# Kernel tuning notes

Hardware: AMD Instinct MI355X
Metric: run time of the kernel (lower is better)

The kernel has to match this reference:

```python
import jax, jax.numpy as jnp
import numpy as np

# Architecture constants from Dense_test.__init__
N_HID = 200      # n
BRANCH = 8
IN_DIM = 120     # 40 * 3
N_OUT = 12
VTH = 1.0        # vth=1, dt=1 -> R*dt factor = 1

# Multi-gaussian surrogate-gradient spike (ActFun_adp from DH-SNN)
LENS, SCALE, HIGHT, GAMMA = 0.5, 6.0, 0.15, 0.5

@jax.custom_vjp
def spike_fn(v):
    return (v > 0).astype(v.dtype)

def _spike_fwd(v):
    return (v > 0).astype(v.dtype), v

def _gauss(x, mu, sigma):
    return jnp.exp(-((x - mu) ** 2) / (2.0 * sigma ** 2)) / (jnp.sqrt(2.0 * jnp.pi) * sigma)

def _spike_bwd(v, g):
    sg = (_gauss(v, 0.0, LENS) * (1.0 + HIGHT)
          - _gauss(v, LENS, SCALE * LENS) * HIGHT
          - _gauss(v, -LENS, SCALE * LENS) * HIGHT)
    return (g * sg * GAMMA,)

spike_fn.defvjp(_spike_fwd, _spike_bwd)


def make_branch_mask(rng, in_features, out_dim, branch):
    # Each output neuron's dendritic branches connect to disjoint random
    # subsets of (input + recurrent) lines.
    k = in_features // branch
    mask = np.zeros((out_dim * branch, in_features), np.float32)
    for i in range(out_dim):
        seq = rng.permutation(in_features)
        for j in range(branch):
            mask[i * branch + j, seq[j * k:(j + 1) * k]] = 1.0
    return jnp.asarray(mask)


def setup_inputs() -> dict:
    rng = np.random.default_rng(0)
    key = jax.random.key(0)
    ks = jax.random.split(key, 16)
    B, T = 1024, 101
    d = {"x": jax.random.normal(ks[0], (B, 3, T, 40), jnp.float32)}
    in_feats = [IN_DIM + N_HID, N_HID + N_HID, N_HID + N_HID]
    for li, in_f in enumerate(in_feats, start=1):
        mask = make_branch_mask(rng, in_f, N_HID, BRANCH)
        W = jax.random.normal(ks[li], (N_HID * BRANCH, in_f), jnp.float32) / np.sqrt(in_f)
        d[f"W{li}"] = W * mask   # mask is applied multiplicatively to dense weights
        d[f"b{li}"] = jnp.zeros((N_HID * BRANCH,), jnp.float32)
        d[f"tau_m{li}"] = jax.random.uniform(ks[li + 4], (N_HID,), jnp.float32, 0.0, 4.0)
        d[f"tau_n{li}"] = jax.random.uniform(ks[li + 8], (N_HID, BRANCH), jnp.float32, 0.0, 4.0)
    d["W4"] = jax.random.normal(ks[12], (N_OUT, N_HID), jnp.float32) / np.sqrt(N_HID)
    d["b4"] = jnp.zeros((N_OUT,), jnp.float32)
    d["tau_m4"] = jax.random.uniform(ks[13], (N_OUT,), jnp.float32, 0.0, 4.0)
    return d


def _forward(x, W1, b1, tau_m1, tau_n1, W2, b2, tau_m2, tau_n2,
             W3, b3, tau_m3, tau_n3, W4, b4, tau_m4):
    B, C, T, F = x.shape
    xs = jnp.transpose(x, (2, 0, 1, 3)).reshape(T, B, C * F)  # [T, B, 120]

    def dense_step(inp, spike, d, mem, W, b, tau_m, tau_n):
        k = jnp.concatenate([inp, spike], axis=1)              # recurrent concat
        ff = (k @ W.T + b).reshape(B, N_HID, BRANCH)
        beta = jax.nn.sigmoid(tau_n)                           # [N_HID, BRANCH]
        d = beta * d + (1.0 - beta) * ff                       # dendritic current
        alpha = jax.nn.sigmoid(tau_m)
        mem = (mem - VTH * spike) * alpha + (1.0 - alpha) * d.sum(-1)
        spike = spike_fn(mem - VTH)
        return spike, d, mem

    z = lambda *s: jnp.zeros(s, x.dtype)
    init = (z(B, N_HID), z(B, N_HID, BRANCH), z(B, N_HID),
            z(B, N_HID), z(B, N_HID, BRANCH), z(B, N_HID),
            z(B, N_HID), z(B, N_HID, BRANCH), z(B, N_HID),
            z(B, N_OUT), z(B, N_OUT))
    alpha4 = jax.nn.sigmoid(tau_m4)

    def step(carry, xt):
        s1, d1, m1, s2, d2, m2, s3, d3, m3, m4, acc = carry
        s1, d1, m1 = dense_step(xt, s1, d1, m1, W1, b1, tau_m1, tau_n1)
        s2, d2, m2 = dense_step(s1, s2, d2, m2, W2, b2, tau_m2, tau_n2)
        s3, d3, m3 = dense_step(s2, s3, d3, m3, W3, b3, tau_m3, tau_n3)
        m4 = m4 * alpha4 + (1.0 - alpha4) * (s3 @ W4.T + b4)   # leaky readout
        acc = acc + m4
        return (s1, d1, m1, s2, d2, m2, s3, d3, m3, m4, acc), None

    carry, _ = jax.lax.scan(step, init, xs)
    acc = carry[-1]
    return jax.nn.log_softmax(acc / T, axis=1)


def reference(x, W1, b1, tau_m1, tau_n1, W2, b2, tau_m2, tau_n2,
              W3, b3, tau_m3, tau_n3, W4, b4, tau_m4):
    return _forward(x, W1, b1, tau_m1, tau_n1, W2, b2, tau_m2, tau_n2,
                    W3, b3, tau_m3, tau_n3, W4, b4, tau_m4)
```

## Files before the change

kernel.cpp:

```cpp
#include <hip/hip_runtime.h>
#include <stdint.h>

#define T_STEPS 101
#define ROWS 1600
#define NTHR 1024
#define NBLK 256
#define NP1 20
#define NP23 25
#define PO2 (NP1 * ROWS)
#define PO3 (PO2 + NP23 * ROWS)
#define NPTOT (PO3 + NP23 * ROWS)

#define W2_OFF 0
#define C2_OFF (NPTOT * 8)
#define BB_OFF (C2_OFF + NPTOT * 4)
#define SA_OFF (BB_OFF + 3 * ROWS * 8)

__device__ __forceinline__ float sigmoidf(float v) { return 1.0f / (1.0f + expf(-v)); }

__global__ void prep_kernel(const float* __restrict__ W1, const float* __restrict__ W2,
                            const float* __restrict__ W3,
                            const float* __restrict__ b1, const float* __restrict__ tn1,
                            const float* __restrict__ tm1,
                            const float* __restrict__ b2, const float* __restrict__ tn2,
                            const float* __restrict__ tm2,
                            const float* __restrict__ b3, const float* __restrict__ tn3,
                            const float* __restrict__ tm3,
                            uint8_t* __restrict__ ws) {
  int gid = blockIdx.x * blockDim.x + threadIdx.x;
  if (gid >= 3 * ROWS) return;
  int l = gid / ROWS, r = gid - l * ROWS;
  const float *W, *bb, *tn, *tm; int in_f, knz, np, poff, scale;
  if (l == 0)      { W = W1; bb = b1; tn = tn1; tm = tm1; in_f = 320; knz = 40; np = NP1;  poff = 0;   scale = 16; }
  else if (l == 1) { W = W2; bb = b2; tn = tn2; tm = tm2; in_f = 400; knz = 50; np = NP23; poff = PO2; scale = 4; }
  else             { W = W3; bb = b3; tn = tn3; tm = tm3; in_f = 400; knz = 50; np = NP23; poff = PO3; scale = 4; }
  float2* w2 = (float2*)(ws + W2_OFF) + poff;
  uint32_t* c2 = (uint32_t*)(ws + C2_OFF) + poff;
  float wl[52]; uint32_t cl[52];
  int cnt = 0;
  for (int col = 0; col < in_f; ++col) {
    float w = W[(size_t)r * in_f + col];
    if (w != 0.0f && cnt < knz) { wl[cnt] = w; cl[cnt] = (uint32_t)(col * scale); ++cnt; }
  }
  for (; cnt < 2 * np; ++cnt) { wl[cnt] = 0.0f; cl[cnt] = 0u; }
  for (int p = 0; p < np; ++p) {
    w2[p * ROWS + r] = make_float2(wl[2 * p], wl[2 * p + 1]);
    c2[p * ROWS + r] = cl[2 * p] | (cl[2 * p + 1] << 16);
  }
  ((float2*)(ws + BB_OFF))[l * ROWS + r] = make_float2(sigmoidf(tn[r]), bb[r]);
  if (r < 200) ((float*)(ws + SA_OFF))[l * 200 + r] = sigmoidf(tm[r]);
}

template<int NP, bool F32, bool WA, bool WB, bool WK1>
__device__ __forceinline__ void slot_compute(
    int tid, int r,
    const float2* __restrict__ w2, const uint32_t* __restrict__ c2,
    const uint8_t* __restrict__ ktab,
    const float2* __restrict__ bbL, const float* __restrict__ saL,
    float (&dreg)[4], uint8_t (*s_l)[4], float (*mem_l)[4],
    uint8_t (*spA)[4], uint8_t (*spB)[4], float4* k1n)
{
  const float2 bb = bbL[r];
  const float bt = bb.x;
  float a0 = bb.y, a1 = bb.y, a2 = bb.y, a3 = bb.y;
  const float2* wp = w2 + r;
  const uint32_t* cp = c2 + r;
#pragma unroll 5
  for (int p = 0; p < NP; ++p) {
    const float2 w = wp[(size_t)p * ROWS];
    const uint32_t c = cp[(size_t)p * ROWS];
    if constexpr (F32) {
      { const float4 kv = *reinterpret_cast<const float4*>(ktab + (c & 0xffffu));
        a0 = fmaf(w.x, kv.x, a0); a1 = fmaf(w.x, kv.y, a1);
        a2 = fmaf(w.x, kv.z, a2); a3 = fmaf(w.x, kv.w, a3); }
      { const float4 kv = *reinterpret_cast<const float4*>(ktab + (c >> 16));
        a0 = fmaf(w.y, kv.x, a0); a1 = fmaf(w.y, kv.y, a1);
        a2 = fmaf(w.y, kv.z, a2); a3 = fmaf(w.y, kv.w, a3); }
    } else {
      { const uint32_t q = *reinterpret_cast<const uint32_t*>(ktab + (c & 0xffffu));
        a0 = fmaf(w.x, (float)(q & 0xffu), a0);
        a1 = fmaf(w.x, (float)((q >> 8) & 0xffu), a1);
        a2 = fmaf(w.x, (float)((q >> 16) & 0xffu), a2);
        a3 = fmaf(w.x, (float)(q >> 24), a3); }
      { const uint32_t q = *reinterpret_cast<const uint32_t*>(ktab + (c >> 16));
        a0 = fmaf(w.y, (float)(q & 0xffu), a0);
        a1 = fmaf(w.y, (float)((q >> 8) & 0xffu), a1);
        a2 = fmaf(w.y, (float)((q >> 16) & 0xffu), a2);
        a3 = fmaf(w.y, (float)(q >> 24), a3); }
    }
  }
  const float ob = 1.0f - bt;
  float d0 = fmaf(bt, dreg[0], ob * a0);
  float d1 = fmaf(bt, dreg[1], ob * a1);
  float d2 = fmaf(bt, dreg[2], ob * a2);
  float d3 = fmaf(bt, dreg[3], ob * a3);
  dreg[0] = d0; dreg[1] = d1; dreg[2] = d2; dreg[3] = d3;
  d0 += __shfl_xor(d0, 1); d0 += __shfl_xor(d0, 2); d0 += __shfl_xor(d0, 4);
  d1 += __shfl_xor(d1, 1); d1 += __shfl_xor(d1, 2); d1 += __shfl_xor(d1, 4);
  d2 += __shfl_xor(d2, 1); d2 += __shfl_xor(d2, 2); d2 += __shfl_xor(d2, 4);
  d3 += __shfl_xor(d3, 1); d3 += __shfl_xor(d3, 2); d3 += __shfl_xor(d3, 4);
  if ((tid & 7) == 0) {
    const int n = r >> 3;
    const float al = saL[n], oa = 1.0f - al;
    float4 mv = *reinterpret_cast<float4*>(&mem_l[n][0]);
    const uint32_t so = *reinterpret_cast<uint32_t*>(&s_l[n][0]);
    const float m0 = fmaf(mv.x - (float)(so & 0xffu),         al, oa * d0);
    const float m1 = fmaf(mv.y - (float)((so >> 8) & 0xffu),  al, oa * d1);
    const float m2 = fmaf(mv.z - (float)((so >> 16) & 0xffu), al, oa * d2);
    const float m3 = fmaf(mv.w - (float)(so >> 24),           al, oa * d3);
    *reinterpret_cast<float4*>(&mem_l[n][0]) = make_float4(m0, m1, m2, m3);
    const uint32_t sn = (m0 > 1.0f ? 1u : 0u) | (m1 > 1.0f ? 0x100u : 0u)
                      | (m2 > 1.0f ? 0x10000u : 0u) | (m3 > 1.0f ? 0x1000000u : 0u);
    *reinterpret_cast<uint32_t*>(&s_l[n][0]) = sn;
    if constexpr (WA) *reinterpret_cast<uint32_t*>(&spA[n][0]) = sn;
    if constexpr (WB) *reinterpret_cast<uint32_t*>(&spB[n][0]) = sn;
    if constexpr (WK1)
      k1n[120 + n] = make_float4(m0 > 1.0f ? 1.0f : 0.0f, m1 > 1.0f ? 1.0f : 0.0f,
                                 m2 > 1.0f ? 1.0f : 0.0f, m3 > 1.0f ? 1.0f : 0.0f);
  }
}

__global__ void __launch_bounds__(NTHR)
snn_main(const float* __restrict__ x,
         const float* __restrict__ W4, const float* __restrict__ b4,
         const float* __restrict__ tm4,
         const float2* __restrict__ w2G, const uint32_t* __restrict__ c2G,
         const float2* __restrict__ bbG, const float* __restrict__ saG,
         float* __restrict__ out)
{
  __shared__ __align__(16) float4   k1f[2][320];
  __shared__ __align__(4)  uint8_t  k2tab[2][400][4];
  __shared__ __align__(4)  uint8_t  k3tab[2][400][4];
  __shared__ __align__(4)  uint8_t  s_lds[3][200][4];
  __shared__ __align__(16) float    mem_lds[3][200][4];
  __shared__ float  w4_lds[12][201];
  __shared__ float2 bbL[3 * ROWS];
  __shared__ float  saL[3 * 200];
  __shared__ float  smx[12][4];

  const int tid = threadIdx.x;
  const int bg  = blockIdx.x;

  for (int idx = tid; idx < 600; idx += NTHR) {
    reinterpret_cast<uint32_t*>(&s_lds[0][0][0])[idx] = 0u;
    reinterpret_cast<float4*>(&mem_lds[0][0][0])[idx] = make_float4(0.f, 0.f, 0.f, 0.f);
  }
  for (int idx = tid; idx < 800; idx += NTHR) {
    reinterpret_cast<uint32_t*>(&k2tab[0][0][0])[idx] = 0u;
    reinterpret_cast<uint32_t*>(&k3tab[0][0][0])[idx] = 0u;
  }
  for (int idx = tid; idx < 200; idx += NTHR)
    k1f[0][120 + idx] = make_float4(0.f, 0.f, 0.f, 0.f);
  for (int idx = tid; idx < 12 * 200; idx += NTHR)
    w4_lds[idx / 200][idx % 200] = W4[idx];
  for (int idx = tid; idx < 3 * ROWS; idx += NTHR) bbL[idx] = bbG[idx];
  for (int idx = tid; idx < 3 * 200; idx += NTHR) saL[idx] = saG[idx];
  if (tid < 480) {
    const int bat = tid / 120, cf = tid - bat * 120;
    const int c = cf / 40, f = cf - c * 40;
    reinterpret_cast<float*>(&k1f[0][cf])[bat] =
        x[(((size_t)(bg * 4 + bat) * 3 + c) * T_STEPS) * 40 + f];
  }

  float d[3][2][4];
#pragma unroll
  for (int l = 0; l < 3; ++l)
#pragma unroll
    for (int i = 0; i < 2; ++i)
#pragma unroll
      for (int b = 0; b < 4; ++b) d[l][i][b] = 0.0f;

  const int r1 = tid + 576;
  float m4_reg = 0.0f, m4_acc = 0.0f, a4 = 0.0f, b4r = 0.0f;
  if (tid < 192) { const int o = tid >> 4; a4 = sigmoidf(tm4[o]); b4r = b4[o]; }
  const float* xpA = nullptr; const float* xpB = nullptr;
  int dofA = 0, dofB = 0;
  if (tid >= 192 && tid < 448) {
    const int q0 = tid - 192;
    { const int bat = q0 / 120, cf = q0 - bat * 120;
      const int c = cf / 40, f = cf - c * 40;
      xpA = x + (((size_t)(bg * 4 + bat) * 3 + c) * T_STEPS) * 40 + f;
      dofA = cf * 4 + bat; }
    const int q1 = q0 + 256;
    if (q1 < 480) {
      const int bat = q1 / 120, cf = q1 - bat * 120;
      const int c = cf / 40, f = cf - c * 40;
      xpB = x + (((size_t)(bg * 4 + bat) * 3 + c) * T_STEPS) * 40 + f;
      dofB = cf * 4 + bat;
    }
  }
  __syncthreads();

  for (int t = 0; t < T_STEPS; ++t) {
    const int cur = t & 1, nxt = cur ^ 1;
    const uint8_t* k1b = reinterpret_cast<const uint8_t*>(&k1f[cur][0]);
    const uint8_t* k2b = reinterpret_cast<const uint8_t*>(&k2tab[cur][0][0]);
    const uint8_t* k3b = reinterpret_cast<const uint8_t*>(&k3tab[cur][0][0]);
    float xv0 = 0.f, xv1 = 0.f;
    const bool doX = (tid >= 192 && tid < 448) && (t + 1 < T_STEPS);
    if (doX) {
      xv0 = xpA[(t + 1) * 40];
      if (xpB) xv1 = xpB[(t + 1) * 40];
    }
    slot_compute<NP1, true, true, false, true>(
        tid, tid, w2G, c2G, k1b, bbL, saL, d[0][0], s_lds[0], mem_lds[0],
        k2tab[cur], k2tab[cur], k1f[nxt]);
    if (tid >= 448) {
      slot_compute<NP1, true, true, false, true>(
          tid, r1, w2G, c2G, k1b, bbL, saL, d[0][1], s_lds[0], mem_lds[0],
          k2tab[cur], k2tab[cur], k1f[nxt]);
    } else if (tid >= 192) {
      if (doX) {
        reinterpret_cast<float*>(&k1f[nxt][0])[dofA] = xv0;
        if (xpB) reinterpret_cast<float*>(&k1f[nxt][0])[dofB] = xv1;
      }
    } else if (t > 0) {
      const int sub = tid & 3, pair = tid >> 2, o = pair >> 4, bat = pair & 3;
      float part = 0.0f;
#pragma unroll 10
      for (int m = 0; m < 50; ++m) {
        const int n = 4 * m + sub;
        part = fmaf(w4_lds[(tid >> 4)][n], (float)s_lds[2][n][(tid >> 2) & 3], part);
      }
      part += __shfl_xor(part, 1);
      part += __shfl_xor(part, 2);
      const float dot = b4r + part;
      m4_reg = a4 * m4_reg + (1.0f - a4) * dot;
      m4_acc += m4_reg;
    }
    __syncthreads();
    slot_compute<NP23, false, true, true, false>(
        tid, tid, w2G + PO2, c2G + PO2, k2b, bbL + ROWS, saL + 200,
        d[1][0], s_lds[1], mem_lds[1], k3tab[cur], k2tab[nxt] + 200, nullptr);
    if (tid >= 448)
      slot_compute<NP23, false, true, true, false>(
          tid, r1, w2G + PO2, c2G + PO2, k2b, bbL + ROWS, saL + 200,
          d[1][1], s_lds[1], mem_lds[1], k3tab[cur], k2tab[nxt] + 200, nullptr);
    __syncthreads();
    slot_compute<NP23, false, false, true, false>(
        tid, tid, w2G + PO3, c2G + PO3, k3b, bbL + 2 * ROWS, saL + 400,
        d[2][0], s_lds[2], mem_lds[2], k3tab[cur], k3tab[nxt] + 200, nullptr);
    if (tid >= 448)
      slot_compute<NP23, false, false, true, false>(
          tid, r1, w2G + PO3, c2G + PO3, k3b, bbL + 2 * ROWS, saL + 400,
          d[2][1], s_lds[2], mem_lds[2], k3tab[cur], k3tab[nxt] + 200, nullptr);
    __syncthreads();
  }

  if (tid < 192) {
    const int sub = tid & 3;
    float part = 0.0f;
#pragma unroll 10
    for (int m = 0; m < 50; ++m) {
      const int n = 4 * m + sub;
      part = fmaf(w4_lds[(tid >> 4)][n], (float)s_lds[2][n][(tid >> 2) & 3], part);
    }
    part += __shfl_xor(part, 1);
    part += __shfl_xor(part, 2);
    const float dot = b4r + part;
    m4_reg = a4 * m4_reg + (1.0f - a4) * dot;
    m4_acc += m4_reg;
    if ((tid & 3) == 0)
      smx[tid >> 4][(tid >> 2) & 3] = m4_acc * (1.0f / (float)T_STEPS);
  }
  __syncthreads();
  if (tid < 4) {
    const int bat = tid;
    float v[12], mx = -1e30f;
#pragma unroll
    for (int o = 0; o < 12; ++o) { v[o] = smx[o][bat]; mx = fmaxf(mx, v[o]); }
    float s = 0.0f;
#pragma unroll
    for (int o = 0; o < 12; ++o) s += expf(v[o] - mx);
    const float ls = logf(s);
#pragma unroll
    for (int o = 0; o < 12; ++o)
      out[((size_t)(bg * 4 + bat)) * 12 + o] = v[o] - mx - ls;
  }
}

extern "C" void kernel_launch(void* const* d_in, const int* in_sizes, int n_in,
                              void* d_out, int out_size, void* d_ws, size_t ws_size,
                              hipStream_t stream) {
  (void)in_sizes; (void)n_in; (void)out_size; (void)ws_size;
  const float* x   = (const float*)d_in[0];
  const float* W1  = (const float*)d_in[1];
  const float* b1  = (const float*)d_in[2];
  const float* tm1 = (const float*)d_in[3];
  const float* tn1 = (const float*)d_in[4];
  const float* W2  = (const float*)d_in[5];
  const float* b2  = (const float*)d_in[6];
  const float* tm2 = (const float*)d_in[7];
  const float* tn2 = (const float*)d_in[8];
  const float* W3  = (const float*)d_in[9];
  const float* b3  = (const float*)d_in[10];
  const float* tm3 = (const float*)d_in[11];
  const float* tn3 = (const float*)d_in[12];
  const float* W4  = (const float*)d_in[13];
  const float* b4  = (const float*)d_in[14];
  const float* tm4 = (const float*)d_in[15];

  uint8_t* ws = (uint8_t*)d_ws;
  const float2*   w2G = (const float2*)(ws + W2_OFF);
  const uint32_t* c2G = (const uint32_t*)(ws + C2_OFF);
  const float2*   bbG = (const float2*)(ws + BB_OFF);
  const float*    saG = (const float*)(ws + SA_OFF);

  prep_kernel<<<dim3(19), dim3(256), 0, stream>>>(
      W1, W2, W3, b1, tn1, tm1, b2, tn2, tm2, b3, tn3, tm3, ws);
  snn_main<<<dim3(NBLK), dim3(NTHR), 0, stream>>>(
      x, W4, b4, tm4, w2G, c2G, bbG, saG, (float*)d_out);
}
```

Measured before the change: 3.147 ms.

## Software-pipeline the three SNN layers across timesteps with one barrier per step

Replaces the per-timestep sequence of three layer phases, each followed by a block barrier, with a wavefront-skewed pipeline. Layer 1 runs step u, layer 2 runs step u-1 and layer 3 runs step u-2, all in the same phase, so each iteration needs only one __syncthreads. Work is now split by wave: 75 wave-sized row slots are spread across 16 waves, two waves load the next x slice directly from global memory, and three waves compute the readout from the layer-3 spike table. The change cuts barrier count and lets layers overlap, but it adds pipeline fill and drain iterations, extra double-buffer indexing and possible load imbalance across waves.

```diff
diff --git a/kernel.cpp b/kernel.cpp
--- a/kernel.cpp
+++ b/kernel.cpp
@@ -139,6 +139,7 @@
   __shared__ float  smx[12][4];
 
   const int tid = threadIdx.x;
+  const int wv  = tid >> 6;
   const int bg  = blockIdx.x;
 
   for (int idx = tid; idx < 600; idx += NTHR) {
@@ -162,106 +163,85 @@
         x[(((size_t)(bg * 4 + bat) * 3 + c) * T_STEPS) * 40 + f];
   }
 
-  float d[3][2][4];
-#pragma unroll
-  for (int l = 0; l < 3; ++l)
-#pragma unroll
-    for (int i = 0; i < 2; ++i)
-#pragma unroll
-      for (int b = 0; b < 4; ++b) d[l][i][b] = 0.0f;
-
-  const int r1 = tid + 576;
+  float d[5][4];
+#pragma unroll
+  for (int k = 0; k < 5; ++k)
+#pragma unroll
+    for (int b = 0; b < 4; ++b) d[k][b] = 0.0f;
+
   float m4_reg = 0.0f, m4_acc = 0.0f, a4 = 0.0f, b4r = 0.0f;
-  if (tid < 192) { const int o = tid >> 4; a4 = sigmoidf(tm4[o]); b4r = b4[o]; }
-  const float* xpA = nullptr; const float* xpB = nullptr;
-  int dofA = 0, dofB = 0;
-  if (tid >= 192 && tid < 448) {
-    const int q0 = tid - 192;
-    { const int bat = q0 / 120, cf = q0 - bat * 120;
-      const int c = cf / 40, f = cf - c * 40;
-      xpA = x + (((size_t)(bg * 4 + bat) * 3 + c) * T_STEPS) * 40 + f;
-      dofA = cf * 4 + bat; }
-    const int q1 = q0 + 256;
-    if (q1 < 480) {
-      const int bat = q1 / 120, cf = q1 - bat * 120;
-      const int c = cf / 40, f = cf - c * 40;
-      xpB = x + (((size_t)(bg * 4 + bat) * 3 + c) * T_STEPS) * 40 + f;
-      dofB = cf * 4 + bat;
+  if (tid >= 704 && tid < 896) {
+    const int o = (tid - 704) >> 4;
+    a4 = sigmoidf(tm4[o]); b4r = b4[o];
+  }
+  __syncthreads();
+
+  const int lane = tid & 63;
+
+  for (int u = 0; u <= T_STEPS + 2; ++u) {
+    const int cur = u & 1, oth = cur ^ 1;
+    const uint8_t* k1b = reinterpret_cast<const uint8_t*>(&k1f[cur][0]);
+    const uint8_t* k2b = reinterpret_cast<const uint8_t*>(&k2tab[oth][0][0]);
+    const uint8_t* k3b = reinterpret_cast<const uint8_t*>(&k3tab[cur][0][0]);
+    const bool runL1 = (u <= T_STEPS - 1);
+    const bool runL2 = (u >= 1 && u <= T_STEPS);
+    const bool runL3 = (u >= 2 && u <= T_STEPS + 1);
+#pragma unroll
+    for (int k = 0; k < 5; ++k) {
+      const int id = wv + 16 * k;
+      if (id >= 75) break;
+      const int layer = id / 25;
+      const int r = (id - layer * 25) * 64 + lane;
+      if (layer == 0) {
+        if (runL1)
+          slot_compute<NP1, true, true, false, true>(
+              tid, r, w2G, c2G, k1b, bbL, saL, d[k], s_lds[0], mem_lds[0],
+              k2tab[cur], k2tab[cur], k1f[oth]);
+      } else if (layer == 1) {
+        if (runL2)
+          slot_compute<NP23, false, true, true, false>(
+              tid, r, w2G + PO2, c2G + PO2, k2b, bbL + ROWS, saL + 200,
+              d[k], s_lds[1], mem_lds[1], k3tab[oth], k2tab[cur] + 200, nullptr);
+      } else {
+        if (runL3)
+          slot_compute<NP23, false, false, true, false>(
+              tid, r, w2G + PO3, c2G + PO3, k3b, bbL + 2 * ROWS, saL + 400,
+              d[k], s_lds[2], mem_lds[2], nullptr, k3tab[oth] + 200, nullptr);
+      }
     }
-  }
-  __syncthreads();
-
-  for (int t = 0; t < T_STEPS; ++t) {
-    const int cur = t & 1, nxt = cur ^ 1;
-    const uint8_t* k1b = reinterpret_cast<const uint8_t*>(&k1f[cur][0]);
-    const uint8_t* k2b = reinterpret_cast<const uint8_t*>(&k2tab[cur][0][0]);
-    const uint8_t* k3b = reinterpret_cast<const uint8_t*>(&k3tab[cur][0][0]);
-    float xv0 = 0.f, xv1 = 0.f;
-    const bool doX = (tid >= 192 && tid < 448) && (t + 1 < T_STEPS);
-    if (doX) {
-      xv0 = xpA[(t + 1) * 40];
-      if (xpB) xv1 = xpB[(t + 1) * 40];
-    }
-    slot_compute<NP1, true, true, false, true>(
-        tid, tid, w2G, c2G, k1b, bbL, saL, d[0][0], s_lds[0], mem_lds[0],
-        k2tab[cur], k2tab[cur], k1f[nxt]);
-    if (tid >= 448) {
-      slot_compute<NP1, true, true, false, true>(
-          tid, r1, w2G, c2G, k1b, bbL, saL, d[0][1], s_lds[0], mem_lds[0],
-          k2tab[cur], k2tab[cur], k1f[nxt]);
-    } else if (tid >= 192) {
-      if (doX) {
-        reinterpret_cast<float*>(&k1f[nxt][0])[dofA] = xv0;
-        if (xpB) reinterpret_cast<float*>(&k1f[nxt][0])[dofB] = xv1;
+    if (wv >= 14) {
+      if (u + 1 <= T_STEPS - 1) {
+        const int rid = tid - 896;
+        for (int e = rid; e < 480; e += 128) {
+          const int bat = e / 120, cf = e - bat * 120;
+          const int c = cf / 40, f = cf - c * 40;
+          reinterpret_cast<float*>(&k1f[oth][cf])[bat] =
+              x[(((size_t)(bg * 4 + bat) * 3 + c) * T_STEPS + (u + 1)) * 40 + f];
+        }
       }
-    } else if (t > 0) {
-      const int sub = tid & 3, pair = tid >> 2, o = pair >> 4, bat = pair & 3;
-      float part = 0.0f;
+    } else if (wv >= 11) {
+      if (u >= 3) {
+        const int rid = tid - 704;
+        const int sub = rid & 3, bat = (rid >> 2) & 3, o = rid >> 4;
+        float part = 0.0f;
 #pragma unroll 10
-      for (int m = 0; m < 50; ++m) {
-        const int n = 4 * m + sub;
-        part = fmaf(w4_lds[(tid >> 4)][n], (float)s_lds[2][n][(tid >> 2) & 3], part);
+        for (int m = 0; m < 50; ++m) {
+          const int n = 4 * m + sub;
+          part = fmaf(w4_lds[o][n], (float)k3tab[cur][200 + n][bat], part);
+        }
+        part += __shfl_xor(part, 1);
+        part += __shfl_xor(part, 2);
+        const float dot = b4r + part;
+        m4_reg = a4 * m4_reg + (1.0f - a4) * dot;
+        m4_acc += m4_reg;
       }
-      part += __shfl_xor(part, 1);
-      part += __shfl_xor(part, 2);
-      const float dot = b4r + part;
-      m4_reg = a4 * m4_reg + (1.0f - a4) * dot;
-      m4_acc += m4_reg;
     }
     __syncthreads();
-    slot_compute<NP23, false, true, true, false>(
-        tid, tid, w2G + PO2, c2G + PO2, k2b, bbL + ROWS, saL + 200,
-        d[1][0], s_lds[1], mem_lds[1], k3tab[cur], k2tab[nxt] + 200, nullptr);
-    if (tid >= 448)
-      slot_compute<NP23, false, true, true, false>(
-          tid, r1, w2G + PO2, c2G + PO2, k2b, bbL + ROWS, saL + 200,
-          d[1][1], s_lds[1], mem_lds[1], k3tab[cur], k2tab[nxt] + 200, nullptr);
-    __syncthreads();
-    slot_compute<NP23, false, false, true, false>(
-        tid, tid, w2G + PO3, c2G + PO3, k3b, bbL + 2 * ROWS, saL + 400,
-        d[2][0], s_lds[2], mem_lds[2], k3tab[cur], k3tab[nxt] + 200, nullptr);
-    if (tid >= 448)
-      slot_compute<NP23, false, false, true, false>(
-          tid, r1, w2G + PO3, c2G + PO3, k3b, bbL + 2 * ROWS, saL + 400,
-          d[2][1], s_lds[2], mem_lds[2], k3tab[cur], k3tab[nxt] + 200, nullptr);
-    __syncthreads();
-  }
-
-  if (tid < 192) {
-    const int sub = tid & 3;
-    float part = 0.0f;
-#pragma unroll 10
-    for (int m = 0; m < 50; ++m) {
-      const int n = 4 * m + sub;
-      part = fmaf(w4_lds[(tid >> 4)][n], (float)s_lds[2][n][(tid >> 2) & 3], part);
-    }
-    part += __shfl_xor(part, 1);
-    part += __shfl_xor(part, 2);
-    const float dot = b4r + part;
-    m4_reg = a4 * m4_reg + (1.0f - a4) * dot;
-    m4_acc += m4_reg;
-    if ((tid & 3) == 0)
-      smx[tid >> 4][(tid >> 2) & 3] = m4_acc * (1.0f / (float)T_STEPS);
+  }
+
+  if (tid >= 704 && tid < 896 && ((tid - 704) & 3) == 0) {
+    const int rid = tid - 704;
+    smx[rid >> 4][(rid >> 2) & 3] = m4_acc * (1.0f / (float)T_STEPS);
   }
   __syncthreads();
   if (tid < 4) {
```

Result: faster. 2.648 ms (-15.9%).
